# Performance work log

Measured on AMD Instinct MI355X. Metric: run time of the kernel, lower is better.

The kernel has to match this reference:

```python
import jax, jax.numpy as jnp
import numpy as np


def setup_inputs() -> dict:
    key = jax.random.key(0)
    k1, k2, k3 = jax.random.split(key, 3)
    B, C, H, W = 256, 1, 512, 512
    SIZE, OUT = 512, 1
    x = jax.random.normal(k1, (B, C, H, W), dtype=jnp.float32)
    weights = jax.random.normal(k2, (SIZE, 4 * C, OUT), dtype=jnp.float32)
    biases = jax.random.normal(k3, (SIZE, OUT), dtype=jnp.float32)
    return {"x": x, "weights": weights, "biases": biases}


def _corner_ring_means(x, size):
    """Mean of the L-shaped ring between the (i)x(i) and (i-1)x(i-1) corner
    squares, for all four corners, computed via a summed-area table.
    Returns [B, size, 4*C] with corner order (tl, tr, bl, br), matching the
    original torch cat along the channel axis."""
    B, C = x.shape[0], x.shape[1]
    idx = jnp.arange(size)

    def corner_square_sums(y):
        # summed-area table anchored at top-left of y
        S = jnp.cumsum(jnp.cumsum(y, axis=2), axis=3)
        # S[..., i-1, i-1] = sum of y[:, :, :i, :i]
        return S[:, :, idx, idx]  # [B, C, size]

    tl = corner_square_sums(x)
    tr = corner_square_sums(x[:, :, :, ::-1])
    bl = corner_square_sums(x[:, :, ::-1, :])
    br = corner_square_sums(x[:, :, ::-1, ::-1])
    sq = jnp.stack([tl, tr, bl, br], axis=-1)  # [B, C, size, 4]

    # ring sum_i = square_sum_i - square_sum_{i-1}
    prev = jnp.concatenate([jnp.zeros_like(sq[:, :, :1]), sq[:, :, :-1]], axis=2)
    # ring pixel count: i*i - (i-1)*(i-1) = 2i - 1
    denom = (2 * jnp.arange(1, size + 1) - 1).astype(x.dtype)
    means = (sq - prev) / denom[None, None, :, None]  # [B, C, size, 4]

    # match torch cat(dim=2) of four [B, size, C] tensors -> [B, size, 4*C]
    return jnp.transpose(means, (0, 2, 3, 1)).reshape(B, size, 4 * C)


def reference(x, weights, biases):
    size = weights.shape[0]
    feats = _corner_ring_means(x, size)               # [B, size, 4]
    # F.linear(x_i, weights[i].T, biases[i]) == x_i @ weights[i] + biases[i]
    out = jnp.einsum('bsf,sfo->bso', feats, weights) + biases[None]
    out = jax.nn.relu(out)                            # per-index activation
    # torch cat(dim=1) of [B, out] chunks then squeeze(-1); out=1 -> [B, size]
    return out.reshape(x.shape[0], -1)
```

## Files before the change

### kernel.cpp

```cpp
#include <hip/hip_runtime.h>


#define HH 512
#define WW 512
#define NRING 512

__global__ __launch_bounds__(256, 4)
void ring_sum_kernel(const float* __restrict__ x, float* __restrict__ rs) {
    __shared__ float bins[4 * NRING];
    const int tid  = threadIdx.x;
    const int lane = tid & 63;
    const int wave = tid >> 6;
    const int b     = blockIdx.x >> 3;
    const int chunk = blockIdx.x & 7;

    for (int t = tid; t < 4 * NRING; t += 256) bins[t] = 0.f;
    __syncthreads();

    float vTL[8] = {0,0,0,0,0,0,0,0};
    float vTR[8] = {0,0,0,0,0,0,0,0};
    float vBL[8] = {0,0,0,0,0,0,0,0};
    float vBR[8] = {0,0,0,0,0,0,0,0};

    const float4* img = (const float4*)x + (size_t)b * (HH * WW / 4);
    const int cA = 4 * lane;
    const int cB = 256 + 4 * lane;

    for (int k = 0; k < 16; ++k) {
        const int r = chunk * 64 + wave * 16 + k;
        const int s = 511 - r;
        const float4* rowp = img + r * (WW / 4);
        float4 a  = rowp[lane];
        float4 bb = rowp[64 + lane];
        float uTL = 0.f, uTR = 0.f, uBL = 0.f, uBR = 0.f;

        if (r < 256) {
            #pragma unroll
            for (int j = 0; j < 4; ++j) {
                float v = (&a.x)[j]; int c = cA + j;
                uBL += v;
                vTR[j] += v;
                float sel  = (c <= r) ? v : 0.f; uTL += sel;  vTL[j] += v - sel;
                float sel2 = (c >= r) ? v : 0.f; uBR += sel2; vBR[j] += v - sel2;
            }
            #pragma unroll
            for (int j = 0; j < 4; ++j) {
                float v = (&bb.x)[j]; int c = cB + j;
                uBR += v;
                vTL[4 + j] += v;
                float sel  = (c >= s) ? v : 0.f; uTR += sel;  vTR[4 + j] += v - sel;
                float sel2 = (c <= s) ? v : 0.f; uBL += sel2; vBL[4 + j] += v - sel2;
            }
        } else {
            #pragma unroll
            for (int j = 0; j < 4; ++j) {
                float v = (&a.x)[j]; int c = cA + j;
                uTL += v;
                vBR[j] += v;
                float sel  = (c >= s) ? v : 0.f; uTR += sel;  vTR[j] += v - sel;
                float sel2 = (c <= s) ? v : 0.f; uBL += sel2; vBL[j] += v - sel2;
            }
            #pragma unroll
            for (int j = 0; j < 4; ++j) {
                float v = (&bb.x)[j]; int c = cB + j;
                uTR += v;
                vBL[4 + j] += v;
                float sel  = (c <= r) ? v : 0.f; uTL += sel;  vTL[4 + j] += v - sel;
                float sel2 = (c >= r) ? v : 0.f; uBR += sel2; vBR[4 + j] += v - sel2;
            }
        }

        for (int off = 32; off > 0; off >>= 1) {
            uTL += __shfl_down(uTL, off);
            uTR += __shfl_down(uTR, off);
            uBL += __shfl_down(uBL, off);
            uBR += __shfl_down(uBR, off);
        }
        if (lane == 0) {
            atomicAdd(&bins[0 * NRING + r], uTL);
            atomicAdd(&bins[1 * NRING + r], uTR);
            atomicAdd(&bins[2 * NRING + s], uBL);
            atomicAdd(&bins[3 * NRING + s], uBR);
        }
    }

    #pragma unroll
    for (int e = 0; e < 8; ++e) {
        int c = (e < 4) ? (cA + e) : (cB + e - 4);
        atomicAdd(&bins[0 * NRING + c],         vTL[e]);
        atomicAdd(&bins[1 * NRING + (511 - c)], vTR[e]);
        atomicAdd(&bins[2 * NRING + c],         vBL[e]);
        atomicAdd(&bins[3 * NRING + (511 - c)], vBR[e]);
    }
    __syncthreads();

    float* out = rs + (size_t)b * (4 * NRING);
    for (int t = tid; t < 4 * NRING; t += 256) {
        int corner = t >> 9;
        int ring   = t & 511;
        atomicAdd(&out[ring * 4 + corner], bins[t]);
    }
}

__global__ __launch_bounds__(256)
void linear_kernel(const float* __restrict__ rs, const float* __restrict__ wts,
                   const float* __restrict__ bias, float* __restrict__ out, int n) {
    int idx = blockIdx.x * 256 + threadIdx.x;
    if (idx >= n) return;
    int i = idx & 511;
    float4 sgm = ((const float4*)rs)[idx];
    float4 w   = ((const float4*)wts)[i];
    float inv  = 1.0f / (float)(2 * i + 1);
    float val  = (sgm.x * w.x + sgm.y * w.y + sgm.z * w.z + sgm.w * w.w) * inv
               + bias[i];
    out[idx] = fmaxf(val, 0.0f);
}

extern "C" void kernel_launch(void* const* d_in, const int* in_sizes, int n_in,
                              void* d_out, int out_size, void* d_ws, size_t ws_size,
                              hipStream_t stream) {
    const float* x    = (const float*)d_in[0];
    const float* wts  = (const float*)d_in[1];
    const float* bias = (const float*)d_in[2];
    float* out = (float*)d_out;

    const int B = in_sizes[0] / (HH * WW);
    float* rs = (float*)d_ws;

    hipMemsetAsync(rs, 0, (size_t)B * 4 * NRING * sizeof(float), stream);

    ring_sum_kernel<<<dim3(B * 8), dim3(256), 0, stream>>>(x, rs);

    const int n = B * NRING;
    linear_kernel<<<dim3((n + 255) / 256), dim3(256), 0, stream>>>(rs, wts, bias, out, n);
}
```

Baseline: 433.9 us.

## Batch row loads, write per-chunk partials, and reduce them in the linear kernel

```diff
diff --git a/kernel.cpp b/kernel.cpp
--- a/kernel.cpp
+++ b/kernel.cpp
@@ -4,17 +4,19 @@
 #define HH 512
 #define WW 512
 #define NRING 512
+#define NB (4 * NRING)
 
+template<bool PARTIALS>
 __global__ __launch_bounds__(256, 4)
-void ring_sum_kernel(const float* __restrict__ x, float* __restrict__ rs) {
-    __shared__ float bins[4 * NRING];
+void ring_sum_kernel(const float* __restrict__ x, float* __restrict__ ws) {
+    __shared__ float bins[NB];
     const int tid  = threadIdx.x;
     const int lane = tid & 63;
     const int wave = tid >> 6;
     const int b     = blockIdx.x >> 3;
     const int chunk = blockIdx.x & 7;
 
-    for (int t = tid; t < 4 * NRING; t += 256) bins[t] = 0.f;
+    for (int t = tid; t < NB; t += 256) bins[t] = 0.f;
     __syncthreads();
 
     float vTL[8] = {0,0,0,0,0,0,0,0};
@@ -26,61 +28,80 @@
     const int cA = 4 * lane;
     const int cB = 256 + 4 * lane;
 
-    for (int k = 0; k < 16; ++k) {
-        const int r = chunk * 64 + wave * 16 + k;
-        const int s = 511 - r;
-        const float4* rowp = img + r * (WW / 4);
-        float4 a  = rowp[lane];
-        float4 bb = rowp[64 + lane];
-        float uTL = 0.f, uTR = 0.f, uBL = 0.f, uBR = 0.f;
+    const int rbase = chunk * 64 + wave * 16;
+    const bool top = (rbase < 256);
 
-        if (r < 256) {
-            #pragma unroll
-            for (int j = 0; j < 4; ++j) {
-                float v = (&a.x)[j]; int c = cA + j;
-                uBL += v;
-                vTR[j] += v;
-                float sel  = (c <= r) ? v : 0.f; uTL += sel;  vTL[j] += v - sel;
-                float sel2 = (c >= r) ? v : 0.f; uBR += sel2; vBR[j] += v - sel2;
+    for (int batch = 0; batch < 2; ++batch) {
+        const int r0 = rbase + batch * 8;
+
+        float4 A[8], Bv[8];
+        #pragma unroll
+        for (int j = 0; j < 8; ++j) {
+            const float4* rowp = img + (size_t)(r0 + j) * (WW / 4);
+            A[j]  = rowp[lane];
+            Bv[j] = rowp[64 + lane];
+        }
+        __builtin_amdgcn_sched_barrier(0);
+
+        float u[32];
+        #pragma unroll
+        for (int j = 0; j < 8; ++j) {
+            const int r = r0 + j;
+            const int s = 511 - r;
+            float uTL = 0.f, uTR = 0.f, uBL = 0.f, uBR = 0.f;
+            if (top) {
+                #pragma unroll
+                for (int e = 0; e < 4; ++e) {
+                    float v = (&A[j].x)[e]; int c = cA + e;
+                    uBL += v;
+                    vTR[e] += v;
+                    float sel  = (c <= r) ? v : 0.f; uTL += sel;  vTL[e] += v - sel;
+                    float sel2 = (c >= r) ? v : 0.f; uBR += sel2; vBR[e] += v - sel2;
+                }
+                #pragma unroll
+                for (int e = 0; e < 4; ++e) {
+                    float v = (&Bv[j].x)[e]; int c = cB + e;
+                    uBR += v;
+                    vTL[4 + e] += v;
+                    float sel  = (c >= s) ? v : 0.f; uTR += sel;  vTR[4 + e] += v - sel;
+                    float sel2 = (c <= s) ? v : 0.f; uBL += sel2; vBL[4 + e] += v - sel2;
+                }
+            } else {
+                #pragma unroll
+                for (int e = 0; e < 4; ++e) {
+                    float v = (&A[j].x)[e]; int c = cA + e;
+                    uTL += v;
+                    vBR[e] += v;
+                    float sel  = (c >= s) ? v : 0.f; uTR += sel;  vTR[e] += v - sel;
+                    float sel2 = (c <= s) ? v : 0.f; uBL += sel2; vBL[e] += v - sel2;
+                }
+                #pragma unroll
+                for (int e = 0; e < 4; ++e) {
+                    float v = (&Bv[j].x)[e]; int c = cB + e;
+                    uTR += v;
+                    vBL[4 + e] += v;
+                    float sel  = (c <= r) ? v : 0.f; uTL += sel;  vTL[4 + e] += v - sel;
+                    float sel2 = (c >= r) ? v : 0.f; uBR += sel2; vBR[4 + e] += v - sel2;
+                }
             }
-            #pragma unroll
-            for (int j = 0; j < 4; ++j) {
-                float v = (&bb.x)[j]; int c = cB + j;
-                uBR += v;
-                vTL[4 + j] += v;
-                float sel  = (c >= s) ? v : 0.f; uTR += sel;  vTR[4 + j] += v - sel;
-                float sel2 = (c <= s) ? v : 0.f; uBL += sel2; vBL[4 + j] += v - sel2;
-            }
-        } else {
-            #pragma unroll
-            for (int j = 0; j < 4; ++j) {
-                float v = (&a.x)[j]; int c = cA + j;
-                uTL += v;
-                vBR[j] += v;
-                float sel  = (c >= s) ? v : 0.f; uTR += sel;  vTR[j] += v - sel;
-                float sel2 = (c <= s) ? v : 0.f; uBL += sel2; vBL[j] += v - sel2;
-            }
-            #pragma unroll
-            for (int j = 0; j < 4; ++j) {
-                float v = (&bb.x)[j]; int c = cB + j;
-                uTR += v;
-                vBL[4 + j] += v;
-                float sel  = (c <= r) ? v : 0.f; uTL += sel;  vTL[4 + j] += v - sel;
-                float sel2 = (c >= r) ? v : 0.f; uBR += sel2; vBR[4 + j] += v - sel2;
-            }
+            u[j * 4 + 0] = uTL; u[j * 4 + 1] = uTR;
+            u[j * 4 + 2] = uBL; u[j * 4 + 3] = uBR;
         }
 
+        #pragma unroll
         for (int off = 32; off > 0; off >>= 1) {
-            uTL += __shfl_down(uTL, off);
-            uTR += __shfl_down(uTR, off);
-            uBL += __shfl_down(uBL, off);
-            uBR += __shfl_down(uBR, off);
+            #pragma unroll
+            for (int q = 0; q < 32; ++q) u[q] += __shfl_down(u[q], off);
         }
         if (lane == 0) {
-            atomicAdd(&bins[0 * NRING + r], uTL);
-            atomicAdd(&bins[1 * NRING + r], uTR);
-            atomicAdd(&bins[2 * NRING + s], uBL);
-            atomicAdd(&bins[3 * NRING + s], uBR);
+            #pragma unroll
+            for (int j = 0; j < 8; ++j) {
+                const int r = r0 + j, s = 511 - r;
+                atomicAdd(&bins[0 * NRING + r], u[j * 4 + 0]);
+                atomicAdd(&bins[1 * NRING + r], u[j * 4 + 1]);
+                atomicAdd(&bins[2 * NRING + s], u[j * 4 + 2]);
+                atomicAdd(&bins[3 * NRING + s], u[j * 4 + 3]);
+            }
         }
     }
 
@@ -94,26 +115,34 @@
     }
     __syncthreads();
 
-    float* out = rs + (size_t)b * (4 * NRING);
-    for (int t = tid; t < 4 * NRING; t += 256) {
-        int corner = t >> 9;
-        int ring   = t & 511;
-        atomicAdd(&out[ring * 4 + corner], bins[t]);
+    if (PARTIALS) {
+        float* outp = ws + ((size_t)b * 8 + chunk) * NB;
+        for (int t = tid; t < NB; t += 256) outp[t] = bins[t];
+    } else {
+        float* outp = ws + (size_t)b * NB;
+        for (int t = tid; t < NB; t += 256) atomicAdd(&outp[t], bins[t]);
     }
 }
 
-__global__ __launch_bounds__(256)
-void linear_kernel(const float* __restrict__ rs, const float* __restrict__ wts,
-                   const float* __restrict__ bias, float* __restrict__ out, int n) {
-    int idx = blockIdx.x * 256 + threadIdx.x;
-    if (idx >= n) return;
-    int i = idx & 511;
-    float4 sgm = ((const float4*)rs)[idx];
-    float4 w   = ((const float4*)wts)[i];
-    float inv  = 1.0f / (float)(2 * i + 1);
-    float val  = (sgm.x * w.x + sgm.y * w.y + sgm.z * w.z + sgm.w * w.w) * inv
-               + bias[i];
-    out[idx] = fmaxf(val, 0.0f);
+__global__ __launch_bounds__(512)
+void linear_kernel(const float* __restrict__ ws, const float* __restrict__ wts,
+                   const float* __restrict__ bias, float* __restrict__ out,
+                   int nparts) {
+    const int b = blockIdx.x;
+    const int i = threadIdx.x;
+    const float* base = ws + (size_t)b * nparts * NB;
+    float s0 = 0.f, s1 = 0.f, s2 = 0.f, s3 = 0.f;
+    for (int p = 0; p < nparts; ++p) {
+        const float* pb = base + (size_t)p * NB;
+        s0 += pb[0 * NRING + i];
+        s1 += pb[1 * NRING + i];
+        s2 += pb[2 * NRING + i];
+        s3 += pb[3 * NRING + i];
+    }
+    float4 w  = ((const float4*)wts)[i];
+    float inv = 1.0f / (float)(2 * i + 1);
+    float val = (s0 * w.x + s1 * w.y + s2 * w.z + s3 * w.w) * inv + bias[i];
+    out[b * NRING + i] = fmaxf(val, 0.0f);
 }
 
 extern "C" void kernel_launch(void* const* d_in, const int* in_sizes, int n_in,
@@ -125,12 +154,15 @@
     float* out = (float*)d_out;
 
     const int B = in_sizes[0] / (HH * WW);
-    float* rs = (float*)d_ws;
+    float* ws = (float*)d_ws;
 
-    hipMemsetAsync(rs, 0, (size_t)B * 4 * NRING * sizeof(float), stream);
-
-    ring_sum_kernel<<<dim3(B * 8), dim3(256), 0, stream>>>(x, rs);
-
-    const int n = B * NRING;
-    linear_kernel<<<dim3((n + 255) / 256), dim3(256), 0, stream>>>(rs, wts, bias, out, n);
+    const size_t need = (size_t)B * 8 * NB * sizeof(float);
+    if (ws_size >= need) {
+        ring_sum_kernel<true><<<dim3(B * 8), dim3(256), 0, stream>>>(x, ws);
+        linear_kernel<<<dim3(B), dim3(512), 0, stream>>>(ws, wts, bias, out, 8);
+    } else {
+        hipMemsetAsync(ws, 0, (size_t)B * NB * sizeof(float), stream);
+        ring_sum_kernel<false><<<dim3(B * 8), dim3(256), 0, stream>>>(x, ws);
+        linear_kernel<<<dim3(B), dim3(512), 0, stream>>>(ws, wts, bias, out, 1);
+    }
 }
```

Result: slower. 606.5 us (+39.8%).
